# Kernel optimization log

Hardware: AMD Instinct MI355X
Metric: run time of the kernel (lower is better)

The kernel has to match this reference:

```python
import jax, jax.numpy as jnp
import numpy as np

B, H, SQ, SKV, D = 4, 16, 1024, 1024, 64


def setup_inputs() -> dict:
    key = jax.random.key(0)
    k1, k2, k3, k4, k5 = jax.random.split(key, 5)
    return {
        "query": jax.random.normal(k1, (B, H, SQ, D), dtype=jnp.float32),
        "keys": jax.random.normal(k2, (B, H, SKV, D), dtype=jnp.float32),
        "values": jax.random.normal(k3, (B, H, SKV, D), dtype=jnp.float32),
        "mask": jax.random.randint(k4, (B, 1, SQ, SKV), 0, 2, dtype=jnp.int32),
        "additional_logits": jax.random.normal(k5, (B, H, SQ, SKV), dtype=jnp.float32),
    }


def reference(query, keys, values, mask, additional_logits):
    # logits = Q K^T + additional_logits, scaled by sqrt(d)
    logits = jnp.einsum("bhqd,bhkd->bhqk", query, keys)
    logits = logits + additional_logits
    logits = logits / jnp.sqrt(jnp.asarray(query.shape[-1], logits.dtype))
    # masked_fill(mask == 0, -1000.0); mask broadcasts over heads
    logits = jnp.where(mask == 0, jnp.asarray(-1000.0, logits.dtype), logits)
    weights = jax.nn.softmax(logits, axis=-1)
    context_vector = jnp.einsum("bhqk,bhkd->bhqd", weights, values)
    return context_vector, weights
```

## Files before the change

kernel.cpp:

```cpp
#include <hip/hip_runtime.h>

#define NB 4
#define NH 16
#define NSQ 1024
#define NSKV 1024
#define ND 64

typedef __attribute__((ext_vector_type(8))) short short8;
typedef __attribute__((ext_vector_type(4))) float f32x4;
typedef __attribute__((ext_vector_type(4))) int int4v;
typedef __attribute__((ext_vector_type(4))) unsigned int uint4v;
typedef __attribute__((ext_vector_type(2))) unsigned int uint2v;

__device__ __forceinline__ unsigned int cvt_pk(float lo, float hi) {
  unsigned int r;
  asm("v_cvt_pk_bf16_f32 %0, %1, %2" : "=v"(r) : "v"(lo), "v"(hi));
  return r;
}
__device__ __forceinline__ float bf2f(unsigned short h) {
  return __uint_as_float(((unsigned int)h) << 16);
}
__device__ __forceinline__ void bar() { __builtin_amdgcn_s_barrier(); }
__device__ __forceinline__ void lgkm0() {
  asm volatile("s_waitcnt lgkmcnt(0)" ::: "memory");
}
__device__ __forceinline__ void pl32(unsigned& a, unsigned& b) {
  asm("v_permlane32_swap_b32 %0, %1" : "+v"(a), "+v"(b));
}
__device__ __forceinline__ void pl16(unsigned& a, unsigned& b) {
  asm("v_permlane16_swap_b32 %0, %1" : "+v"(a), "+v"(b));
}

__global__ __launch_bounds__(512, 2)
void attn_fused(const float* __restrict__ Q, const float* __restrict__ K,
                const float* __restrict__ V, const int* __restrict__ M,
                const float* __restrict__ A, float* __restrict__ Octx,
                float* __restrict__ Ow)
{
  __shared__ unsigned short Ps[64 * 1024];
  __shared__ __align__(16) unsigned char Stg[18432];
  __shared__ float SumS[64][2];

  const int t  = threadIdx.x;
  const int w  = t >> 6;
  const int l  = t & 63;
  const int lg = l >> 4;
  const int lm = l & 15;
  const int p  = w & 3;
  const int h  = w >> 2;
  const int g  = p * 64 + l;

  const int bid = blockIdx.x;
  const int y   = bid >> 3;
  const int qt  = y & 15;
  const int bh  = (bid & 7) * 8 + (y >> 4);
  const int b   = bh >> 4;
  const int q0  = qt * 64;
  const int kvb = h * 512;

  unsigned char* KsB = Stg + h * 4096;
  unsigned char* VtB = Stg + 8192 + h * 5120;

  const float* Qp = Q + (size_t)bh * NSQ * ND;
  const float* Kp = K + (size_t)bh * NSKV * ND;
  const float* Vp = V + (size_t)bh * NSKV * ND;
  const float* Ap = A + (size_t)bh * NSQ * NSKV;
  const int*   Mp = M + (size_t)b  * NSQ * NSKV;

  const float C = 0.18033688011112042f;

  short8 qf[2];
  {
    const float* qr = Qp + (size_t)(q0 + p * 16 + lm) * ND + lg * 8;
    #pragma unroll
    for (int dc = 0; dc < 2; ++dc) {
      f32x4 x = *(const f32x4*)(qr + dc * 32);
      f32x4 y2 = *(const f32x4*)(qr + dc * 32 + 4);
      uint4v u;
      u[0] = cvt_pk(x[0], x[1]); u[1] = cvt_pk(x[2], x[3]);
      u[2] = cvt_pk(y2[0], y2[1]); u[3] = cvt_pk(y2[2], y2[3]);
      qf[dc] = __builtin_bit_cast(short8, u);
    }
  }

  f32x4 ctx[4];
  #pragma unroll
  for (int i = 0; i < 4; ++i) ctx[i] = (f32x4){0.f, 0.f, 0.f, 0.f};
  float sum = 0.f;

  f32x4 sk[2], sv[2];
  f32x4 aA[2], aB[2];  int4v mA[2], mB[2];

  auto issueStage = [&](int c) {
    int kv0 = kvb + c * 32;
    const float* kb = Kp + (size_t)kv0 * ND + g * 4;
    const float* vb = Vp + (size_t)kv0 * ND + g * 4;
    sk[0] = *(const f32x4*)kb;       sk[1] = *(const f32x4*)(kb + 1024);
    sv[0] = *(const f32x4*)vb;       sv[1] = *(const f32x4*)(vb + 1024);
  };
  auto loadAM = [&](int c, f32x4* a, int4v* m) {
    int kv0 = kvb + c * 32;
    #pragma unroll
    for (int sub = 0; sub < 2; ++sub) {
      size_t off = (size_t)(q0 + p * 16 + lm) * NSKV + kv0 + sub * 16 + lg * 4;
      a[sub] = *(const f32x4*)(Ap + off);
      m[sub] = *(const int4v*)(Mp + off);
    }
  };
  auto writeStage = [&]() {
    #pragma unroll
    for (int i = 0; i < 2; ++i) {
      int f = g * 4 + i * 1024;
      int row = f >> 6;
      int cb  = (f & 63) * 2;
      uint2v u;
      u[0] = cvt_pk(sk[i][0], sk[i][1]);
      u[1] = cvt_pk(sk[i][2], sk[i][3]);
      *(uint2v*)(KsB + row * 128 + (cb ^ ((row & 7) << 4))) = u;
    }
    #pragma unroll
    for (int i = 0; i < 2; ++i) {
      unsigned r0 = __float_as_uint(sv[i][0]);
      unsigned r1 = __float_as_uint(sv[i][1]);
      unsigned r2 = __float_as_uint(sv[i][2]);
      unsigned r3 = __float_as_uint(sv[i][3]);
      pl32(r0, r2); pl32(r1, r3);
      pl16(r0, r1); pl16(r2, r3);
      int d = 4 * (l & 15) + (l >> 4);
      int kvbase = 4 * p + 16 * i;
      uint2v vu;
      vu[0] = cvt_pk(__uint_as_float(r0), __uint_as_float(r1));
      vu[1] = cvt_pk(__uint_as_float(r2), __uint_as_float(r3));
      *(uint2v*)(VtB + d * 80 + ((kvbase * 2) ^ (((d >> 2) & 3) << 4))) = vu;
    }
  };

  auto compute = [&](int c, const f32x4* a, const int4v* m) {
    int kv0 = kvb + c * 32;
    const int ksw = (lm & 7) << 4;
    const int vsw = ((lm >> 2) & 3) << 4;
    short8 kf[4];
    #pragma unroll
    for (int sub = 0; sub < 2; ++sub)
      #pragma unroll
      for (int dc = 0; dc < 2; ++dc)
        kf[sub * 2 + dc] = *(const short8*)(
            KsB + (sub * 16 + lm) * 128 + ((dc * 64 + lg * 16) ^ ksw));
    short8 vf[4];
    #pragma unroll
    for (int ds = 0; ds < 4; ++ds)
      vf[ds] = *(const short8*)(VtB + (ds * 16 + lm) * 80 + ((lg * 16) ^ vsw));

    __builtin_amdgcn_s_setprio(1);
    unsigned s0, s1, s2, s3;
    {
      f32x4 acc = (f32x4){0.f, 0.f, 0.f, 0.f};
      acc = __builtin_amdgcn_mfma_f32_16x16x32_bf16(kf[0], qf[0], acc, 0, 0, 0);
      acc = __builtin_amdgcn_mfma_f32_16x16x32_bf16(kf[1], qf[1], acc, 0, 0, 0);
      float pe[4];
      #pragma unroll
      for (int j = 0; j < 4; ++j) {
        float amc = m[0][j] ? a[0][j] * C : -1.8e8f;
        pe[j] = exp2f(fmaf(acc[j], C, amc));
        sum += pe[j];
      }
      s0 = cvt_pk(pe[0], pe[1]); s1 = cvt_pk(pe[2], pe[3]);
      uint2v u2; u2[0] = s0; u2[1] = s1;
      *(uint2v*)((char*)Ps + (p * 16 + lm) * 2048 +
                 (((kv0 + lg * 4) * 2) ^ (lm << 4))) = u2;
    }
    {
      f32x4 acc = (f32x4){0.f, 0.f, 0.f, 0.f};
      acc = __builtin_amdgcn_mfma_f32_16x16x32_bf16(kf[2], qf[0], acc, 0, 0, 0);
      acc = __builtin_amdgcn_mfma_f32_16x16x32_bf16(kf[3], qf[1], acc, 0, 0, 0);
      float pe[4];
      #pragma unroll
      for (int j = 0; j < 4; ++j) {
        float amc = m[1][j] ? a[1][j] * C : -1.8e8f;
        pe[j] = exp2f(fmaf(acc[j], C, amc));
        sum += pe[j];
      }
      s2 = cvt_pk(pe[0], pe[1]); s3 = cvt_pk(pe[2], pe[3]);
      uint2v u2; u2[0] = s2; u2[1] = s3;
      *(uint2v*)((char*)Ps + (p * 16 + lm) * 2048 +
                 (((kv0 + 16 + lg * 4) * 2) ^ (lm << 4))) = u2;
    }
    pl32(s0, s2); pl32(s1, s3);
    pl16(s0, s2); pl16(s1, s3);
    uint4v pu; pu[0] = s0; pu[1] = s1; pu[2] = s2; pu[3] = s3;
    short8 pf = __builtin_bit_cast(short8, pu);
    #pragma unroll
    for (int ds = 0; ds < 4; ++ds)
      ctx[ds] = __builtin_amdgcn_mfma_f32_16x16x32_bf16(pf, vf[ds], ctx[ds], 0, 0, 0);
    __builtin_amdgcn_s_setprio(0);
  };

  issueStage(0);
  loadAM(0, aA, mA);
  if (h == 1) {
    writeStage();
    issueStage(1);
    loadAM(1, aB, mB);
  }
  lgkm0(); bar();

  for (int c = 0; c < 16; c += 2) {
    int n1 = (c + 1 > 15) ? 15 : c + 1;
    int n2 = (c + 2 > 15) ? 15 : c + 2;
    int n3 = (c + 3 > 15) ? 15 : c + 3;
    if (h == 0) { writeStage(); issueStage(n1); loadAM(n1, aB, mB); }
    else        { compute(c, aA, mA); }
    lgkm0(); bar();
    if (h == 0) { compute(c, aA, mA); }
    else        { writeStage(); issueStage(n2); loadAM(n2, aA, mA); }
    lgkm0(); bar();
    if (h == 0) { writeStage(); issueStage(n2); loadAM(n2, aA, mA); }
    else        { compute(c + 1, aB, mB); }
    lgkm0(); bar();
    if (h == 0) { compute(c + 1, aB, mB); }
    else        { writeStage(); issueStage(n3); loadAM(n3, aB, mB); }
    lgkm0(); bar();
  }

  sum += __shfl_xor(sum, 16);
  sum += __shfl_xor(sum, 32);
  if (lg == 0) SumS[p * 16 + lm][h] = sum;
  lgkm0(); bar();

  float (*CtxS)[16][64] = (float(*)[16][64])Stg;
  if (h == 1) {
    #pragma unroll
    for (int ds = 0; ds < 4; ++ds)
      #pragma unroll
      for (int j = 0; j < 4; ++j)
        CtxS[p][lg * 4 + j][ds * 16 + lm] = ctx[ds][j];
  }
  lgkm0(); bar();

  if (h == 0) {
    float rcpj[4];
    #pragma unroll
    for (int j = 0; j < 4; ++j) {
      int r = p * 16 + lg * 4 + j;
      rcpj[j] = 1.0f / (SumS[r][0] + SumS[r][1]);
    }
    #pragma unroll
    for (int ds = 0; ds < 4; ++ds)
      #pragma unroll
      for (int j = 0; j < 4; ++j)
        Octx[((size_t)bh * NSQ + q0 + p * 16 + lg * 4 + j) * ND + ds * 16 + lm] =
            (ctx[ds][j] + CtxS[p][lg * 4 + j][ds * 16 + lm]) * rcpj[j];
  }

  float* Owp = Ow + (size_t)bh * NSQ * NSKV + (size_t)(q0 + p * 16) * NSKV;
  for (int r = 0; r < 16; ++r) {
    float rr = 1.0f / (SumS[p * 16 + r][0] + SumS[p * 16 + r][1]);
    int kv = kvb + l * 8;
    short8 pv = *(const short8*)((char*)Ps + (p * 16 + r) * 2048 +
                                 ((kv * 2) ^ (r << 4)));
    f32x4 o1, o2;
    o1[0] = bf2f((unsigned short)pv[0]) * rr;
    o1[1] = bf2f((unsigned short)pv[1]) * rr;
    o1[2] = bf2f((unsigned short)pv[2]) * rr;
    o1[3] = bf2f((unsigned short)pv[3]) * rr;
    o2[0] = bf2f((unsigned short)pv[4]) * rr;
    o2[1] = bf2f((unsigned short)pv[5]) * rr;
    o2[2] = bf2f((unsigned short)pv[6]) * rr;
    o2[3] = bf2f((unsigned short)pv[7]) * rr;
    *(f32x4*)&Owp[(size_t)r * NSKV + kv]     = o1;
    *(f32x4*)&Owp[(size_t)r * NSKV + kv + 4] = o2;
  }
}

extern "C" void kernel_launch(void* const* d_in, const int* in_sizes, int n_in,
                              void* d_out, int out_size, void* d_ws, size_t ws_size,
                              hipStream_t stream) {
  const float* Q = (const float*)d_in[0];
  const float* K = (const float*)d_in[1];
  const float* V = (const float*)d_in[2];
  const int*   M = (const int*)d_in[3];
  const float* A = (const float*)d_in[4];
  float* ctx = (float*)d_out;
  float* wts = ctx + (size_t)NB * NH * NSQ * ND;
  dim3 grid(NB * NH * (NSQ / 64));
  attn_fused<<<grid, dim3(512), 0, stream>>>(Q, K, V, M, A, ctx, wts);
}
```

Before: 183.9 us.

## Double KV chunk size to 64 and pre-fold mask into scaled logits on load

Each pipeline stage now covers 64 KV rows instead of 32, so the loop runs 8 chunks with half as many barriers, and the K/V staging buffers grow to 16KB per half with a row pitch of 128 bytes and an XOR swizzle. The mask and additional-logit inputs are merged into a single scaled bias when they are loaded, which drops the separate mask registers and the select from the compute path. The epilogue reuses the staging buffer for the row sums and the context partials and merges one barrier. The cost is more registers for the larger prefetch (4 f32x4 each for K, V and A) and more LDS, which may reduce occupancy at launch_bounds(512,2).

```diff
diff --git a/kernel.cpp b/kernel.cpp
--- a/kernel.cpp
+++ b/kernel.cpp
@@ -38,8 +38,7 @@
                 float* __restrict__ Ow)
 {
   __shared__ unsigned short Ps[64 * 1024];
-  __shared__ __align__(16) unsigned char Stg[18432];
-  __shared__ float SumS[64][2];
+  __shared__ __align__(16) unsigned char Stg[32768];
 
   const int t  = threadIdx.x;
   const int w  = t >> 6;
@@ -58,8 +57,8 @@
   const int q0  = qt * 64;
   const int kvb = h * 512;
 
-  unsigned char* KsB = Stg + h * 4096;
-  unsigned char* VtB = Stg + 8192 + h * 5120;
+  unsigned char* KsB = Stg + h * 16384;
+  unsigned char* VtB = KsB + 8192;
 
   const float* Qp = Q + (size_t)bh * NSQ * ND;
   const float* Kp = K + (size_t)bh * NSKV * ND;
@@ -88,28 +87,35 @@
   for (int i = 0; i < 4; ++i) ctx[i] = (f32x4){0.f, 0.f, 0.f, 0.f};
   float sum = 0.f;
 
-  f32x4 sk[2], sv[2];
-  f32x4 aA[2], aB[2];  int4v mA[2], mB[2];
+  f32x4 sk[4], sv[4];
+  f32x4 aA[4], aB[4];
 
   auto issueStage = [&](int c) {
-    int kv0 = kvb + c * 32;
+    int kv0 = kvb + c * 64;
     const float* kb = Kp + (size_t)kv0 * ND + g * 4;
     const float* vb = Vp + (size_t)kv0 * ND + g * 4;
-    sk[0] = *(const f32x4*)kb;       sk[1] = *(const f32x4*)(kb + 1024);
-    sv[0] = *(const f32x4*)vb;       sv[1] = *(const f32x4*)(vb + 1024);
-  };
-  auto loadAM = [&](int c, f32x4* a, int4v* m) {
-    int kv0 = kvb + c * 32;
-    #pragma unroll
-    for (int sub = 0; sub < 2; ++sub) {
+    #pragma unroll
+    for (int i = 0; i < 4; ++i) {
+      sk[i] = *(const f32x4*)(kb + i * 1024);
+      sv[i] = *(const f32x4*)(vb + i * 1024);
+    }
+  };
+  auto loadAF = [&](int c, f32x4* a) {
+    int kv0 = kvb + c * 64;
+    #pragma unroll
+    for (int sub = 0; sub < 4; ++sub) {
       size_t off = (size_t)(q0 + p * 16 + lm) * NSKV + kv0 + sub * 16 + lg * 4;
-      a[sub] = *(const f32x4*)(Ap + off);
-      m[sub] = *(const int4v*)(Mp + off);
+      f32x4 av = *(const f32x4*)(Ap + off);
+      int4v mv = *(const int4v*)(Mp + off);
+      f32x4 r;
+      #pragma unroll
+      for (int j = 0; j < 4; ++j) r[j] = mv[j] ? av[j] * C : -1.8e8f;
+      a[sub] = r;
     }
   };
   auto writeStage = [&]() {
     #pragma unroll
-    for (int i = 0; i < 2; ++i) {
+    for (int i = 0; i < 4; ++i) {
       int f = g * 4 + i * 1024;
       int row = f >> 6;
       int cb  = (f & 63) * 2;
@@ -117,9 +123,6 @@
       u[0] = cvt_pk(sk[i][0], sk[i][1]);
       u[1] = cvt_pk(sk[i][2], sk[i][3]);
       *(uint2v*)(KsB + row * 128 + (cb ^ ((row & 7) << 4))) = u;
-    }
-    #pragma unroll
-    for (int i = 0; i < 2; ++i) {
       unsigned r0 = __float_as_uint(sv[i][0]);
       unsigned r1 = __float_as_uint(sv[i][1]);
       unsigned r2 = __float_as_uint(sv[i][2]);
@@ -131,103 +134,107 @@
       uint2v vu;
       vu[0] = cvt_pk(__uint_as_float(r0), __uint_as_float(r1));
       vu[1] = cvt_pk(__uint_as_float(r2), __uint_as_float(r3));
-      *(uint2v*)(VtB + d * 80 + ((kvbase * 2) ^ (((d >> 2) & 3) << 4))) = vu;
-    }
-  };
-
-  auto compute = [&](int c, const f32x4* a, const int4v* m) {
-    int kv0 = kvb + c * 32;
+      *(uint2v*)(VtB + d * 128 + ((kvbase * 2) ^ ((d & 7) << 4))) = vu;
+    }
+  };
+
+  auto compute = [&](int c, const f32x4* a) {
+    int kv0 = kvb + c * 64;
     const int ksw = (lm & 7) << 4;
-    const int vsw = ((lm >> 2) & 3) << 4;
-    short8 kf[4];
-    #pragma unroll
-    for (int sub = 0; sub < 2; ++sub)
-      #pragma unroll
-      for (int dc = 0; dc < 2; ++dc)
-        kf[sub * 2 + dc] = *(const short8*)(
-            KsB + (sub * 16 + lm) * 128 + ((dc * 64 + lg * 16) ^ ksw));
-    short8 vf[4];
-    #pragma unroll
-    for (int ds = 0; ds < 4; ++ds)
-      vf[ds] = *(const short8*)(VtB + (ds * 16 + lm) * 80 + ((lg * 16) ^ vsw));
-
     __builtin_amdgcn_s_setprio(1);
-    unsigned s0, s1, s2, s3;
-    {
-      f32x4 acc = (f32x4){0.f, 0.f, 0.f, 0.f};
-      acc = __builtin_amdgcn_mfma_f32_16x16x32_bf16(kf[0], qf[0], acc, 0, 0, 0);
-      acc = __builtin_amdgcn_mfma_f32_16x16x32_bf16(kf[1], qf[1], acc, 0, 0, 0);
-      float pe[4];
-      #pragma unroll
-      for (int j = 0; j < 4; ++j) {
-        float amc = m[0][j] ? a[0][j] * C : -1.8e8f;
-        pe[j] = exp2f(fmaf(acc[j], C, amc));
-        sum += pe[j];
+    #pragma unroll
+    for (int kh = 0; kh < 2; ++kh) {
+      short8 kf[4];
+      #pragma unroll
+      for (int sj = 0; sj < 2; ++sj)
+        #pragma unroll
+        for (int dc = 0; dc < 2; ++dc)
+          kf[sj * 2 + dc] = *(const short8*)(
+              KsB + ((kh * 2 + sj) * 16 + lm) * 128 + ((dc * 64 + lg * 16) ^ ksw));
+      short8 vf[4];
+      #pragma unroll
+      for (int ds = 0; ds < 4; ++ds)
+        vf[ds] = *(const short8*)(
+            VtB + (ds * 16 + lm) * 128 + ((kh * 64 + lg * 16) ^ ksw));
+
+      unsigned s0, s1, s2, s3;
+      {
+        const int sub = kh * 2;
+        f32x4 acc = (f32x4){0.f, 0.f, 0.f, 0.f};
+        acc = __builtin_amdgcn_mfma_f32_16x16x32_bf16(kf[0], qf[0], acc, 0, 0, 0);
+        acc = __builtin_amdgcn_mfma_f32_16x16x32_bf16(kf[1], qf[1], acc, 0, 0, 0);
+        float pe[4];
+        #pragma unroll
+        for (int j = 0; j < 4; ++j) {
+          pe[j] = exp2f(fmaf(acc[j], C, a[sub][j]));
+          sum += pe[j];
+        }
+        s0 = cvt_pk(pe[0], pe[1]); s1 = cvt_pk(pe[2], pe[3]);
+        uint2v u2; u2[0] = s0; u2[1] = s1;
+        *(uint2v*)((char*)Ps + (p * 16 + lm) * 2048 +
+                   (((kv0 + kh * 32 + lg * 4) * 2) ^ (lm << 4))) = u2;
       }
-      s0 = cvt_pk(pe[0], pe[1]); s1 = cvt_pk(pe[2], pe[3]);
-      uint2v u2; u2[0] = s0; u2[1] = s1;
-      *(uint2v*)((char*)Ps + (p * 16 + lm) * 2048 +
-                 (((kv0 + lg * 4) * 2) ^ (lm << 4))) = u2;
-    }
-    {
-      f32x4 acc = (f32x4){0.f, 0.f, 0.f, 0.f};
-      acc = __builtin_amdgcn_mfma_f32_16x16x32_bf16(kf[2], qf[0], acc, 0, 0, 0);
-      acc = __builtin_amdgcn_mfma_f32_16x16x32_bf16(kf[3], qf[1], acc, 0, 0, 0);
-      float pe[4];
-      #pragma unroll
-      for (int j = 0; j < 4; ++j) {
-        float amc = m[1][j] ? a[1][j] * C : -1.8e8f;
-        pe[j] = exp2f(fmaf(acc[j], C, amc));
-        sum += pe[j];
+      {
+        const int sub = kh * 2 + 1;
+        f32x4 acc = (f32x4){0.f, 0.f, 0.f, 0.f};
+        acc = __builtin_amdgcn_mfma_f32_16x16x32_bf16(kf[2], qf[0], acc, 0, 0, 0);
+        acc = __builtin_amdgcn_mfma_f32_16x16x32_bf16(kf[3], qf[1], acc, 0, 0, 0);
+        float pe[4];
+        #pragma unroll
+        for (int j = 0; j < 4; ++j) {
+          pe[j] = exp2f(fmaf(acc[j], C, a[sub][j]));
+          sum += pe[j];
+        }
+        s2 = cvt_pk(pe[0], pe[1]); s3 = cvt_pk(pe[2], pe[3]);
+        uint2v u2; u2[0] = s2; u2[1] = s3;
+        *(uint2v*)((char*)Ps + (p * 16 + lm) * 2048 +
+                   (((kv0 + kh * 32 + 16 + lg * 4) * 2) ^ (lm << 4))) = u2;
       }
-      s2 = cvt_pk(pe[0], pe[1]); s3 = cvt_pk(pe[2], pe[3]);
-      uint2v u2; u2[0] = s2; u2[1] = s3;
-      *(uint2v*)((char*)Ps + (p * 16 + lm) * 2048 +
-                 (((kv0 + 16 + lg * 4) * 2) ^ (lm << 4))) = u2;
-    }
-    pl32(s0, s2); pl32(s1, s3);
-    pl16(s0, s2); pl16(s1, s3);
-    uint4v pu; pu[0] = s0; pu[1] = s1; pu[2] = s2; pu[3] = s3;
-    short8 pf = __builtin_bit_cast(short8, pu);
-    #pragma unroll
-    for (int ds = 0; ds < 4; ++ds)
-      ctx[ds] = __builtin_amdgcn_mfma_f32_16x16x32_bf16(pf, vf[ds], ctx[ds], 0, 0, 0);
+      pl32(s0, s2); pl32(s1, s3);
+      pl16(s0, s2); pl16(s1, s3);
+      uint4v pu; pu[0] = s0; pu[1] = s1; pu[2] = s2; pu[3] = s3;
+      short8 pf = __builtin_bit_cast(short8, pu);
+      #pragma unroll
+      for (int ds = 0; ds < 4; ++ds)
+        ctx[ds] = __builtin_amdgcn_mfma_f32_16x16x32_bf16(pf, vf[ds], ctx[ds], 0, 0, 0);
+    }
     __builtin_amdgcn_s_setprio(0);
   };
 
   issueStage(0);
-  loadAM(0, aA, mA);
+  loadAF(0, aA);
   if (h == 1) {
     writeStage();
     issueStage(1);
-    loadAM(1, aB, mB);
+    loadAF(1, aB);
   }
   lgkm0(); bar();
 
-  for (int c = 0; c < 16; c += 2) {
-    int n1 = (c + 1 > 15) ? 15 : c + 1;
-    int n2 = (c + 2 > 15) ? 15 : c + 2;
-    int n3 = (c + 3 > 15) ? 15 : c + 3;
-    if (h == 0) { writeStage(); issueStage(n1); loadAM(n1, aB, mB); }
-    else        { compute(c, aA, mA); }
-    lgkm0(); bar();
-    if (h == 0) { compute(c, aA, mA); }
-    else        { writeStage(); issueStage(n2); loadAM(n2, aA, mA); }
-    lgkm0(); bar();
-    if (h == 0) { writeStage(); issueStage(n2); loadAM(n2, aA, mA); }
-    else        { compute(c + 1, aB, mB); }
-    lgkm0(); bar();
-    if (h == 0) { compute(c + 1, aB, mB); }
-    else        { writeStage(); issueStage(n3); loadAM(n3, aB, mB); }
+  for (int c = 0; c < 8; c += 2) {
+    int n1 = (c + 1 > 7) ? 7 : c + 1;
+    int n2 = (c + 2 > 7) ? 7 : c + 2;
+    int n3 = (c + 3 > 7) ? 7 : c + 3;
+    if (h == 0) { writeStage(); issueStage(n1); loadAF(n1, aB); }
+    else        { compute(c, aA); }
+    lgkm0(); bar();
+    if (h == 0) { compute(c, aA); }
+    else        { writeStage(); issueStage(n2); loadAF(n2, aA); }
+    lgkm0(); bar();
+    if (h == 0) { writeStage(); issueStage(n2); loadAF(n2, aA); }
+    else        { compute(c + 1, aB); }
+    lgkm0(); bar();
+    if (h == 0) { compute(c + 1, aB); }
+    else        { writeStage(); issueStage(n3); loadAF(n3, aB); }
     lgkm0(); bar();
   }
 
   sum += __shfl_xor(sum, 16);
   sum += __shfl_xor(sum, 32);
+  __syncthreads();
+
+  float (*SumS)[2]     = (float(*)[2])Stg;
+  float (*CtxS)[16][64] = (float(*)[16][64])(Stg + 1024);
   if (lg == 0) SumS[p * 16 + lm][h] = sum;
-  lgkm0(); bar();
-
-  float (*CtxS)[16][64] = (float(*)[16][64])Stg;
   if (h == 1) {
     #pragma unroll
     for (int ds = 0; ds < 4; ++ds)
@@ -235,7 +242,7 @@
       for (int j = 0; j < 4; ++j)
         CtxS[p][lg * 4 + j][ds * 16 + lm] = ctx[ds][j];
   }
-  lgkm0(); bar();
+  __syncthreads();
 
   if (h == 0) {
     float rcpj[4];
```

Result: no change. 183.7 us (-0.1%).

## Double-buffer K/V staging so both wave halves compute each phase

Applied to the files above, without the earlier changes.

Replaces the ping-pong schedule, where one half of the waves staged K/V while the other computed, with per-half double-buffered LDS staging. Every wave now writes the next stage, issues loads and computes in the same phase, which halves the barriers per chunk. The mask select is folded into the additive-logit load so the inner loop only does an FMA and exp2, and the V tile pitch drops from 80 to 64 bytes with a new swizzle. LDS use grows (staging from 18 KB to 32 KB), which may limit occupancy at two blocks per CU, and the new V swizzle may introduce bank conflicts.

```diff
diff --git a/kernel.cpp b/kernel.cpp
--- a/kernel.cpp
+++ b/kernel.cpp
@@ -38,8 +38,7 @@
                 float* __restrict__ Ow)
 {
   __shared__ unsigned short Ps[64 * 1024];
-  __shared__ __align__(16) unsigned char Stg[18432];
-  __shared__ float SumS[64][2];
+  __shared__ __align__(16) unsigned char Stg[32768];
 
   const int t  = threadIdx.x;
   const int w  = t >> 6;
@@ -58,9 +57,6 @@
   const int q0  = qt * 64;
   const int kvb = h * 512;
 
-  unsigned char* KsB = Stg + h * 4096;
-  unsigned char* VtB = Stg + 8192 + h * 5120;
-
   const float* Qp = Q + (size_t)bh * NSQ * ND;
   const float* Kp = K + (size_t)bh * NSKV * ND;
   const float* Vp = V + (size_t)bh * NSKV * ND;
@@ -89,7 +85,7 @@
   float sum = 0.f;
 
   f32x4 sk[2], sv[2];
-  f32x4 aA[2], aB[2];  int4v mA[2], mB[2];
+  f32x4 aA[2], aB[2];
 
   auto issueStage = [&](int c) {
     int kv0 = kvb + c * 32;
@@ -98,16 +94,22 @@
     sk[0] = *(const f32x4*)kb;       sk[1] = *(const f32x4*)(kb + 1024);
     sv[0] = *(const f32x4*)vb;       sv[1] = *(const f32x4*)(vb + 1024);
   };
-  auto loadAM = [&](int c, f32x4* a, int4v* m) {
+  auto loadAF = [&](int c, f32x4* a) {
     int kv0 = kvb + c * 32;
     #pragma unroll
     for (int sub = 0; sub < 2; ++sub) {
       size_t off = (size_t)(q0 + p * 16 + lm) * NSKV + kv0 + sub * 16 + lg * 4;
-      a[sub] = *(const f32x4*)(Ap + off);
-      m[sub] = *(const int4v*)(Mp + off);
-    }
-  };
-  auto writeStage = [&]() {
+      f32x4 av = *(const f32x4*)(Ap + off);
+      int4v mv = *(const int4v*)(Mp + off);
+      f32x4 r;
+      #pragma unroll
+      for (int j = 0; j < 4; ++j) r[j] = mv[j] ? av[j] * C : -1.8e8f;
+      a[sub] = r;
+    }
+  };
+  auto writeStage = [&](int buf) {
+    unsigned char* KsB = Stg + h * 16384 + buf * 8192;
+    unsigned char* VtB = KsB + 4096;
     #pragma unroll
     for (int i = 0; i < 2; ++i) {
       int f = g * 4 + i * 1024;
@@ -117,9 +119,6 @@
       u[0] = cvt_pk(sk[i][0], sk[i][1]);
       u[1] = cvt_pk(sk[i][2], sk[i][3]);
       *(uint2v*)(KsB + row * 128 + (cb ^ ((row & 7) << 4))) = u;
-    }
-    #pragma unroll
-    for (int i = 0; i < 2; ++i) {
       unsigned r0 = __float_as_uint(sv[i][0]);
       unsigned r1 = __float_as_uint(sv[i][1]);
       unsigned r2 = __float_as_uint(sv[i][2]);
@@ -131,14 +130,16 @@
       uint2v vu;
       vu[0] = cvt_pk(__uint_as_float(r0), __uint_as_float(r1));
       vu[1] = cvt_pk(__uint_as_float(r2), __uint_as_float(r3));
-      *(uint2v*)(VtB + d * 80 + ((kvbase * 2) ^ (((d >> 2) & 3) << 4))) = vu;
-    }
-  };
-
-  auto compute = [&](int c, const f32x4* a, const int4v* m) {
+      *(uint2v*)(VtB + d * 64 + ((kvbase * 2) ^ (((d >> 1) & 3) << 4))) = vu;
+    }
+  };
+
+  auto compute = [&](int c, int buf, const f32x4* a) {
+    const unsigned char* KsB = Stg + h * 16384 + buf * 8192;
+    const unsigned char* VtB = KsB + 4096;
     int kv0 = kvb + c * 32;
     const int ksw = (lm & 7) << 4;
-    const int vsw = ((lm >> 2) & 3) << 4;
+    const int vsw = ((lm >> 1) & 3) << 4;
     short8 kf[4];
     #pragma unroll
     for (int sub = 0; sub < 2; ++sub)
@@ -149,7 +150,7 @@
     short8 vf[4];
     #pragma unroll
     for (int ds = 0; ds < 4; ++ds)
-      vf[ds] = *(const short8*)(VtB + (ds * 16 + lm) * 80 + ((lg * 16) ^ vsw));
+      vf[ds] = *(const short8*)(VtB + (ds * 16 + lm) * 64 + ((lg * 16) ^ vsw));
 
     __builtin_amdgcn_s_setprio(1);
     unsigned s0, s1, s2, s3;
@@ -160,8 +161,7 @@
       float pe[4];
       #pragma unroll
       for (int j = 0; j < 4; ++j) {
-        float amc = m[0][j] ? a[0][j] * C : -1.8e8f;
-        pe[j] = exp2f(fmaf(acc[j], C, amc));
+        pe[j] = exp2f(fmaf(acc[j], C, a[0][j]));
         sum += pe[j];
       }
       s0 = cvt_pk(pe[0], pe[1]); s1 = cvt_pk(pe[2], pe[3]);
@@ -176,8 +176,7 @@
       float pe[4];
       #pragma unroll
       for (int j = 0; j < 4; ++j) {
-        float amc = m[1][j] ? a[1][j] * C : -1.8e8f;
-        pe[j] = exp2f(fmaf(acc[j], C, amc));
+        pe[j] = exp2f(fmaf(acc[j], C, a[1][j]));
         sum += pe[j];
       }
       s2 = cvt_pk(pe[0], pe[1]); s3 = cvt_pk(pe[2], pe[3]);
@@ -196,38 +195,34 @@
   };
 
   issueStage(0);
-  loadAM(0, aA, mA);
-  if (h == 1) {
-    writeStage();
-    issueStage(1);
-    loadAM(1, aB, mB);
-  }
+  loadAF(0, aA);
+  writeStage(0);
+  issueStage(1);
+  loadAF(1, aB);
   lgkm0(); bar();
 
   for (int c = 0; c < 16; c += 2) {
-    int n1 = (c + 1 > 15) ? 15 : c + 1;
     int n2 = (c + 2 > 15) ? 15 : c + 2;
     int n3 = (c + 3 > 15) ? 15 : c + 3;
-    if (h == 0) { writeStage(); issueStage(n1); loadAM(n1, aB, mB); }
-    else        { compute(c, aA, mA); }
+    writeStage(1);
+    issueStage(n2);
+    compute(c, 0, aA);
+    loadAF(n2, aA);
     lgkm0(); bar();
-    if (h == 0) { compute(c, aA, mA); }
-    else        { writeStage(); issueStage(n2); loadAM(n2, aA, mA); }
-    lgkm0(); bar();
-    if (h == 0) { writeStage(); issueStage(n2); loadAM(n2, aA, mA); }
-    else        { compute(c + 1, aB, mB); }
-    lgkm0(); bar();
-    if (h == 0) { compute(c + 1, aB, mB); }
-    else        { writeStage(); issueStage(n3); loadAM(n3, aB, mB); }
+    writeStage(0);
+    issueStage(n3);
+    compute(c + 1, 1, aB);
+    loadAF(n3, aB);
     lgkm0(); bar();
   }
 
   sum += __shfl_xor(sum, 16);
   sum += __shfl_xor(sum, 32);
+  __syncthreads();
+
+  float (*SumS)[2]      = (float(*)[2])Stg;
+  float (*CtxS)[16][64] = (float(*)[16][64])(Stg + 1024);
   if (lg == 0) SumS[p * 16 + lm][h] = sum;
-  lgkm0(); bar();
-
-  float (*CtxS)[16][64] = (float(*)[16][64])Stg;
   if (h == 1) {
     #pragma unroll
     for (int ds = 0; ds < 4; ++ds)
@@ -235,7 +230,7 @@
       for (int j = 0; j < 4; ++j)
         CtxS[p][lg * 4 + j][ds * 16 + lm] = ctx[ds][j];
   }
-  lgkm0(); bar();
+  __syncthreads();
 
   if (h == 0) {
     float rcpj[4];
```

After: 174.4 us. 5.2% less time.
